# Kernel tuning notes

Measured on AMD Instinct MI355X. Metric: run time of the kernel, lower is better.

The kernel has to match this reference:

```python
import jax, jax.numpy as jnp
import numpy as np

B, T, D = 1, 2048, 2048
NH, DH, DRH, DC = 16, 128, 64, 512


def setup_inputs() -> dict:
    key = jax.random.key(0)
    ks = jax.random.split(key, 12)
    p = lambda k, s: jax.random.normal(k, s, jnp.float32) * 0.02
    h = jax.random.normal(ks[0], (B, T, D), jnp.float32)
    # rotation angles; reference builds complex freqs_cis = cos + i*sin
    freqs_cis = jax.random.uniform(ks[1], (T, DRH // 2), jnp.float32, 0.0, 2.0 * np.pi)
    causal = jnp.tril(jnp.ones((T, T), bool))
    mask = jnp.where(causal, 0.0, -1e9).astype(jnp.float32)
    return {
        "h": h,
        "freqs_cis": freqs_cis,
        "mask": mask,
        "w_dkv": p(ks[2], (DC, D)),
        "w_uk": p(ks[3], (DH, NH, DC)),
        "w_uv": p(ks[4], (DH, NH, DC)),
        "w_dq": p(ks[5], (DC, D)),
        "w_uq": p(ks[6], (DH, NH, DC)),
        "w_qr": p(ks[7], (DRH, NH, DC)),
        "w_kr": p(ks[8], (DRH, D)),
        "w_o": p(ks[9], (D, DH, NH)),
    }


def _rope(x, fc):
    # x: [..., t, drh]; fc: complex [t, drh//2] (broadcasts over leading dims)
    real, imag = jnp.split(x.astype(jnp.float32), 2, -1)
    z = (real + 1j * imag) * fc
    return jnp.concatenate((z.real, z.imag), -1).astype(x.dtype)


def reference(h, freqs_cis, mask, w_dkv, w_uk, w_uv, w_dq, w_uq, w_qr, w_kr, w_o):
    nh, dh, drh = w_uk.shape[1], w_uk.shape[0], w_qr.shape[0]
    fc = jnp.cos(freqs_cis) + 1j * jnp.sin(freqs_cis)  # [t, drh//2] complex
    c_kv = jnp.einsum('cd,btd->btc', w_dkv, h)          # kv latent [b,t,dc]
    k_c = jnp.einsum('enc,btc->bnte', w_uk, c_kv)       # [b,nh,t,dh]
    v_c = jnp.einsum('enc,btc->bnte', w_uv, c_kv)       # [b,nh,t,dh]
    c_q = jnp.einsum('cd,btd->btc', w_dq, h)            # q latent [b,t,dc]
    q_c = jnp.einsum('enc,btc->bnte', w_uq, c_q)        # [b,nh,t,dh]
    q_r = _rope(jnp.einsum('rnc,btc->bntr', w_qr, c_q), fc)  # [b,nh,t,drh]
    k_r = _rope(jnp.einsum('rd,btd->btr', w_kr, h), fc)      # [b,t,drh]
    q = jnp.concatenate((q_c, q_r), -1)                 # [b,nh,t,dh+drh]
    b, t = k_r.shape[0], k_r.shape[1]
    k_r = jnp.broadcast_to(k_r[:, None], (b, nh, t, drh)) / nh
    k = jnp.concatenate((k_c, k_r), -1)                 # [b,nh,t,dh+drh]
    logits = jnp.einsum('bntd,bnld->bntl', q, k) / jnp.sqrt(jnp.float32(dh + drh)) + mask
    scores = jax.nn.softmax(logits.astype(jnp.float32), -1).astype(h.dtype)
    # NOTE: faithful to source: contraction is over the query axis t, output axis is l
    out = jnp.einsum('bntl,bnte->bnle', scores, v_c)    # [b,nh,t,dh] (t named l in src)
    return jnp.einsum('den,bnle->bld', w_o, out)        # [b,t,d]
```

## Files before the change

### kernel.cpp

```cpp
#include <hip/hip_runtime.h>
#include <hip/hip_bf16.h>
#include <math.h>


namespace {

constexpr int T   = 2048;
constexpr int D   = 2048;
constexpr int NH  = 16;
constexpr int DH  = 128;
constexpr int DRH = 64;
constexpr int DC  = 512;
constexpr int QK  = 192;
constexpr float SCL2E = 0.07216878364870322f * 1.4426950408889634f;

constexpr long long PH = 2048LL * 32 * 33;

typedef __attribute__((ext_vector_type(8))) short short8;
typedef __attribute__((ext_vector_type(4))) float f32x4;

#define MFMA16(a, b, c) __builtin_amdgcn_mfma_f32_16x16x32_bf16((a), (b), (c), 0, 0, 0)

__device__ __forceinline__ unsigned short f2b(float x) {
    unsigned u = __float_as_uint(x);
    unsigned r = (u + 0x7FFFu + ((u >> 16) & 1u)) >> 16;
    return (unsigned short)r;
}
__device__ __forceinline__ unsigned short f2bt(float x) {
    return (unsigned short)(__float_as_uint(x) >> 16);
}
__device__ __forceinline__ float b2f(unsigned short s) {
    return __uint_as_float(((unsigned)s) << 16);
}

typedef __attribute__((address_space(1))) const unsigned int* gas_t;
typedef __attribute__((address_space(3))) unsigned int* las_t;
__device__ __forceinline__ void async16(const unsigned short* g, unsigned short* l) {
    __builtin_amdgcn_global_load_lds((gas_t)(const void*)g, (las_t)(void*)l, 16, 0, 0);
}

constexpr long long SZ_H    = (long long)T * D;
constexpr long long SZ_DKV  = (long long)DC * D;
constexpr long long SZ_UK   = (long long)DH * NH * DC;
constexpr long long SZ_UV   = SZ_UK;
constexpr long long SZ_DQ   = SZ_DKV;
constexpr long long SZ_UQ   = SZ_UK;
constexpr long long SZ_QR   = (long long)DRH * NH * DC;
constexpr long long SZ_KR   = (long long)DRH * D;
constexpr long long C0 = SZ_H;
constexpr long long C1 = C0 + SZ_DKV;
constexpr long long C2 = C1 + SZ_UK;
constexpr long long C3 = C2 + SZ_UV;
constexpr long long C4 = C3 + SZ_DQ;
constexpr long long C5 = C4 + SZ_UQ;
constexpr long long C6 = C5 + SZ_QR;
constexpr long long C7 = C6 + SZ_KR;

__global__ __launch_bounds__(256) void cast_all(
    const float* __restrict__ h,   const float* __restrict__ wdkv,
    const float* __restrict__ wuk, const float* __restrict__ wuv,
    const float* __restrict__ wdq, const float* __restrict__ wuq,
    const float* __restrict__ wqr, const float* __restrict__ wkr,
    unsigned short* __restrict__ hb,   unsigned short* __restrict__ dkvb,
    unsigned short* __restrict__ dqb,  unsigned short* __restrict__ ukb,
    unsigned short* __restrict__ uvb,  unsigned short* __restrict__ wqall,
    unsigned short* __restrict__ krb)
{
    long long i4 = ((long long)blockIdx.x * 256 + threadIdx.x) * 4;
    const float* src; unsigned short* dst; long long soff, doff;
    if      (i4 < C0) { src = h;    dst = hb;   soff = i4;      doff = soff; }
    else if (i4 < C1) { src = wdkv; dst = dkvb; soff = i4 - C0; doff = soff; }
    else if (i4 < C2) { src = wuk;  dst = ukb;  soff = i4 - C1; doff = soff; }
    else if (i4 < C3) { src = wuv;  dst = uvb;  soff = i4 - C2; doff = soff; }
    else if (i4 < C4) { src = wdq;  dst = dqb;  soff = i4 - C3; doff = soff; }
    else if (i4 < C5) {
        src = wuq; dst = wqall; soff = i4 - C4;
        long long e = soff >> 13, n = (soff >> 9) & 15, c = soff & 511;
        doff = n * 98304 + e * 512 + c;
    }
    else if (i4 < C6) {
        src = wqr; dst = wqall; soff = i4 - C5;
        long long e = soff >> 13, n = (soff >> 9) & 15, c = soff & 511;
        doff = n * 98304 + (128 + e) * 512 + c;
    }
    else              { src = wkr;  dst = krb;  soff = i4 - C6; doff = soff; }
    float4 v = *(const float4*)(src + soff);
    uint2 pk;
    pk.x = (unsigned)f2b(v.x) | ((unsigned)f2b(v.y) << 16);
    pk.y = (unsigned)f2b(v.z) | ((unsigned)f2b(v.w) << 16);
    *(uint2*)(dst + doff) = pk;
}

__global__ __launch_bounds__(256) void wo_permute(const float* __restrict__ wo,
                                                  unsigned short* __restrict__ wob)
{
    __shared__ float row[2048];
    int d = blockIdx.x;
    const float* src = wo + (long long)d * 2048;
#pragma unroll
    for (int i = 0; i < 8; ++i) row[threadIdx.x + i * 256] = src[threadIdx.x + i * 256];
    __syncthreads();
    unsigned short* dst = wob + (long long)d * 2048;
#pragma unroll
    for (int i = 0; i < 8; ++i) {
        int j = threadIdx.x + i * 256;
        int n = j >> 7, e = j & 127;
        dst[j] = f2b(row[e * 16 + n]);
    }
}

template<int BM, int BN, int WM, int WN, bool OUTB, bool SPLITK = false>
__global__ __launch_bounds__(256) void gemm_bf16(
    const unsigned short* __restrict__ A, const unsigned short* __restrict__ B,
    void* __restrict__ C, int K, int lda, int ldb, int ldc,
    long long sB, long long sC)
{
    constexpr int MT = WM / 16, NT = WN / 16;
    constexpr int WX = BN / WN;
    __shared__ unsigned short As[2][BM * 32];
    __shared__ unsigned short Bs[2][BN * 32];
    const int tid = (int)threadIdx.x;
    const int wave = tid >> 6, lane = tid & 63;
    const int q = lane >> 4, c = lane & 15;
    const int wm = (wave / WX) * WM, wn = (wave % WX) * WN;
    const int m0 = (int)blockIdx.x * BM, n0 = (int)blockIdx.y * BN;

    const unsigned short* Ab;
    const unsigned short* Bb;
    long long cb;
    if constexpr (SPLITK) {
        int koff = (int)blockIdx.z * K;
        Ab = A + koff;
        Bb = B + koff;
        cb = (long long)blockIdx.z * sC;
    } else {
        Ab = A;
        Bb = B + (long long)blockIdx.z * sB;
        cb = (long long)blockIdx.z * sC;
    }

    f32x4 acc[MT][NT];
#pragma unroll
    for (int i = 0; i < MT; ++i)
#pragma unroll
        for (int j = 0; j < NT; ++j) acc[i][j] = (f32x4){0.f, 0.f, 0.f, 0.f};

    auto STAGE = [&](int buf, int k0) {
#pragma unroll
        for (int i = 0; i < BM / 64; ++i) {
            int ch = tid + i * 256;
            async16(&Ab[(long long)(m0 + (ch >> 2)) * lda + k0 + (((ch & 3) ^ ((ch >> 3) & 3)) * 8)],
                    &As[buf][(i * 256 + wave * 64) * 8]);
        }
#pragma unroll
        for (int i = 0; i < BN / 64; ++i) {
            int ch = tid + i * 256;
            async16(&Bb[(long long)(n0 + (ch >> 2)) * ldb + k0 + (((ch & 3) ^ ((ch >> 3) & 3)) * 8)],
                    &Bs[buf][(i * 256 + wave * 64) * 8]);
        }
    };

    STAGE(0, 0);
    __syncthreads();
    int cur = 0;
    for (int k0 = 0; k0 < K; k0 += 32) {
        if (k0 + 32 < K) STAGE(cur ^ 1, k0 + 32);
        short8 af[MT], bfr[NT];
#pragma unroll
        for (int i = 0; i < MT; ++i) {
            int row = wm + i * 16 + c;
            af[i] = *(const short8*)&As[cur][row * 32 + (q ^ ((row >> 1) & 3)) * 8];
        }
#pragma unroll
        for (int j = 0; j < NT; ++j) {
            int row = wn + j * 16 + c;
            bfr[j] = *(const short8*)&Bs[cur][row * 32 + (q ^ ((row >> 1) & 3)) * 8];
        }
#pragma unroll
        for (int i = 0; i < MT; ++i)
#pragma unroll
            for (int j = 0; j < NT; ++j)
                acc[i][j] = MFMA16(af[i], bfr[j], acc[i][j]);
        __syncthreads();
        cur ^= 1;
    }
#pragma unroll
    for (int i = 0; i < MT; ++i)
#pragma unroll
        for (int j = 0; j < NT; ++j) {
            int rbase = m0 + wm + i * 16 + q * 4;
            int col = n0 + wn + j * 16 + c;
#pragma unroll
            for (int rr = 0; rr < 4; ++rr) {
                long long off = cb + (long long)(rbase + rr) * ldc + col;
                if (OUTB) ((unsigned short*)C)[off] = f2b(acc[i][j][rr]);
                else      ((float*)C)[off] = acc[i][j][rr];
            }
        }
}

__global__ __launch_bounds__(256) void rope_q(unsigned short* __restrict__ qh,
                                              const float* __restrict__ fr)
{
    int idx = (int)blockIdx.x * 256 + (int)threadIdx.x;
    int j = idx & 31;
    int t = (idx >> 5) & (T - 1);
    int n = idx >> 16;
    float sn, cs;
    sincosf(fr[t * 32 + j], &sn, &cs);
    long long base = ((long long)(n * T + t)) * QK + 128 + j;
    float x0 = b2f(qh[base]);
    float x1 = b2f(qh[base + 32]);
    qh[base]      = f2b(x0 * cs - x1 * sn);
    qh[base + 32] = f2b(x0 * sn + x1 * cs);
}

__global__ __launch_bounds__(256) void rope_k(const float* __restrict__ krtp,
                                              unsigned short* __restrict__ kh,
                                              const float* __restrict__ fr)
{
    int idx = (int)blockIdx.x * 256 + (int)threadIdx.x;
    int j = idx & 31;
    int t = idx >> 5;
    float sn, cs;
    sincosf(fr[t * 32 + j], &sn, &cs);
    float x0 = 0.f, x1 = 0.f;
#pragma unroll
    for (int pth = 0; pth < 4; ++pth) {
        x0 += krtp[pth * (T * 64) + t * 64 + j];
        x1 += krtp[pth * (T * 64) + t * 64 + 32 + j];
    }
    unsigned short y0 = f2b((x0 * cs - x1 * sn) * (1.0f / 16.0f));
    unsigned short y1 = f2b((x0 * sn + x1 * cs) * (1.0f / 16.0f));
#pragma unroll
    for (int n = 0; n < NH; ++n) {
        long long base = ((long long)(n * T + t)) * QK + 128 + j;
        kh[base]      = y0;
        kh[base + 32] = y1;
    }
}

__global__ __launch_bounds__(256) void vtrans(const unsigned short* __restrict__ vbh,
                                              const float* __restrict__ zrow,
                                              unsigned short* __restrict__ vt)
{
    __shared__ unsigned short ts[32][33];
    __shared__ float zi[32];
    int t0 = (int)blockIdx.x * 32, e0 = (int)blockIdx.y * 32, n = (int)blockIdx.z;
    int tid = (int)threadIdx.x;
    if (tid < 32) zi[tid] = 1.0f / zrow[n * T + t0 + tid];
    int r = tid >> 3, cq = (tid & 7) * 4;
    const unsigned short* src = vbh + ((long long)(n * T + t0 + r)) * DH + e0 + cq;
#pragma unroll
    for (int i = 0; i < 4; ++i) ts[r][cq + i] = src[i];
    __syncthreads();
    unsigned short* dst = vt + ((long long)(n * DH + e0 + r)) * T + t0 + cq;
#pragma unroll
    for (int i = 0; i < 4; ++i) dst[i] = f2b(b2f(ts[cq + i][r]) * zi[cq + i]);
}

__global__ __launch_bounds__(256) void row_stats_p(const unsigned short* __restrict__ qh,
                                                   const unsigned short* __restrict__ kh,
                                                   float* __restrict__ zrow,
                                                   unsigned short* __restrict__ Pbuf)
{
    int id = (int)blockIdx.x;
    int n = (id & 7) * 2 + ((id >> 3) & 1);
    int rest = id >> 4;
    int tbi = 31 - (rest & 31);
    int chunk = rest >> 5;
    int tid = (int)threadIdx.x, wave = tid >> 6, lane = tid & 63;
    int q = lane >> 4, c = lane & 15;
    int tw = tbi * 64 + wave * 16;

    __shared__ unsigned short Ks[64 * 200];

    const unsigned short* qp = qh + ((long long)(n * T + tw + c)) * QK;
    short8 qf[6];
#pragma unroll
    for (int f = 0; f < 6; ++f) qf[f] = *(const short8*)(qp + f * 32 + q * 8);

    float z = 0.f;
    const unsigned short* kbase = kh + (long long)n * T * QK;
    unsigned short* Ph = Pbuf + (long long)n * PH;

    short8 kreg[6];
    int lt = chunk;
    if (lt <= tbi) {
        const unsigned short* kp = kbase + (long long)lt * 64 * QK;
#pragma unroll
        for (int i = 0; i < 6; ++i) {
            int ch = tid + i * 256;
            int r = ch / 24, cc = ch - r * 24;
            kreg[i] = *(const short8*)(kp + r * QK + cc * 8);
        }
    }
    for (; lt <= tbi; lt += 4) {
        __syncthreads();
#pragma unroll
        for (int i = 0; i < 6; ++i) {
            int ch = tid + i * 256;
            int r = ch / 24, cc = ch - r * 24;
            *(short8*)&Ks[r * 200 + cc * 8] = kreg[i];
        }
        __syncthreads();
        if (lt + 4 <= tbi) {
            const unsigned short* kp = kbase + (long long)(lt + 4) * 64 * QK;
#pragma unroll
            for (int i = 0; i < 6; ++i) {
                int ch = tid + i * 256;
                int r = ch / 24, cc = ch - r * 24;
                kreg[i] = *(const short8*)(kp + r * QK + cc * 8);
            }
        }
        f32x4 d[4];
#pragma unroll
        for (int ls = 0; ls < 4; ++ls) d[ls] = (f32x4){0.f, 0.f, 0.f, 0.f};
        __builtin_amdgcn_s_setprio(1);
#pragma unroll
        for (int f = 0; f < 6; ++f)
#pragma unroll
            for (int ls = 0; ls < 4; ++ls) {
                short8 ka = *(const short8*)&Ks[(ls * 16 + c) * 200 + f * 32 + q * 8];
                d[ls] = MFMA16(ka, qf[f], d[ls]);
            }
        __builtin_amdgcn_s_setprio(0);
        int L = T - lt * 64;
        unsigned short* pb = Ph + (long long)2048 * lt * (65 - lt)
                             + (long long)(q * 4) * L + (tbi - lt) * 64 + wave * 16 + c;
        if (lt == tbi) {
            int tl = wave * 16 + c;
#pragma unroll
            for (int ls = 0; ls < 4; ++ls)
#pragma unroll
                for (int r = 0; r < 4; ++r) {
                    float pe = exp2f(d[ls][r] * SCL2E);
                    bool ok = (ls * 16 + q * 4 + r) <= tl;
                    z += ok ? pe : 0.f;
                    pb[(ls * 16 + r) * L] = ok ? f2bt(pe) : (unsigned short)0;
                }
        } else {
#pragma unroll
            for (int ls = 0; ls < 4; ++ls)
#pragma unroll
                for (int r = 0; r < 4; ++r) {
                    float pe = exp2f(d[ls][r] * SCL2E);
                    z += pe;
                    pb[(ls * 16 + r) * L] = f2bt(pe);
                }
        }
    }
    z += __shfl_xor(z, 16);
    z += __shfl_xor(z, 32);
    if (q == 0) atomicAdd(&zrow[n * T + tw + c], z);
}

__global__ __launch_bounds__(256) void pv_gemm(const unsigned short* __restrict__ Pbuf,
                                               const unsigned short* __restrict__ vt,
                                               unsigned short* __restrict__ p0,
                                               unsigned short* __restrict__ p1)
{
    __shared__ unsigned short As[2][64 * 32];
    __shared__ unsigned short Bs[2][128 * 32];
    const int j = (int)blockIdx.x, chunk = (int)blockIdx.y, n = (int)blockIdx.z;
    const int tid = (int)threadIdx.x, wave = tid >> 6, lane = tid & 63;
    const int q = lane >> 4, c = lane & 15;
    const int wm = (wave >> 1) * 32, wn = (wave & 1) * 64;
    const int m0 = j * 64;
    const int L = T - m0;
    const int ntile = 32 - j;
    const unsigned short* A = Pbuf + (long long)n * PH + (long long)2048 * j * (65 - j);
    const unsigned short* B = vt + (long long)n * DH * T + m0;

    f32x4 acc[2][4];
#pragma unroll
    for (int i = 0; i < 2; ++i)
#pragma unroll
        for (int jj = 0; jj < 4; ++jj) acc[i][jj] = (f32x4){0.f, 0.f, 0.f, 0.f};

    const int tcount = (ntile - chunk + 1) >> 1;
    const int nsteps = tcount * 2;

    auto STAGE = [&](int buf, int k0) {
        async16(&A[(long long)(tid >> 2) * L + k0 + (((tid & 3) ^ ((tid >> 3) & 3)) * 8)],
                &As[buf][wave * 512]);
#pragma unroll
        for (int i = 0; i < 2; ++i) {
            int ch = tid + i * 256;
            async16(&B[(long long)(ch >> 2) * T + k0 + (((ch & 3) ^ ((ch >> 3) & 3)) * 8)],
                    &Bs[buf][(i * 256 + wave * 64) * 8]);
        }
    };
    auto K0 = [&](int s) { return (chunk + ((s >> 1) << 1)) * 64 + (s & 1) * 32; };

    if (nsteps > 0) STAGE(0, K0(0));
    __syncthreads();
    int cur = 0;
    for (int s = 0; s < nsteps; ++s) {
        if (s + 1 < nsteps) STAGE(cur ^ 1, K0(s + 1));
        short8 af[2], bfr[4];
#pragma unroll
        for (int i = 0; i < 2; ++i) {
            int row = wm + i * 16 + c;
            af[i] = *(const short8*)&As[cur][row * 32 + (q ^ ((row >> 1) & 3)) * 8];
        }
#pragma unroll
        for (int jj = 0; jj < 4; ++jj) {
            int row = wn + jj * 16 + c;
            bfr[jj] = *(const short8*)&Bs[cur][row * 32 + (q ^ ((row >> 1) & 3)) * 8];
        }
#pragma unroll
        for (int i = 0; i < 2; ++i)
#pragma unroll
            for (int jj = 0; jj < 4; ++jj)
                acc[i][jj] = MFMA16(af[i], bfr[jj], acc[i][jj]);
        __syncthreads();
        cur ^= 1;
    }
    unsigned short* op = chunk ? p1 : p0;
#pragma unroll
    for (int i = 0; i < 2; ++i)
#pragma unroll
        for (int jj = 0; jj < 4; ++jj) {
            int rbase = m0 + wm + i * 16 + q * 4;
            int col = n * 128 + wn + jj * 16 + c;
#pragma unroll
            for (int rr = 0; rr < 4; ++rr)
                op[(long long)(rbase + rr) * D + col] = f2b(acc[i][jj][rr]);
        }
}

__global__ __launch_bounds__(256) void sum_cast2(const unsigned short* __restrict__ a,
                                                 const unsigned short* __restrict__ b,
                                                 unsigned short* __restrict__ o)
{
    long long i = ((long long)blockIdx.x * 256 + threadIdx.x) * 8;
    short8 va = *(const short8*)(a + i);
    short8 vb = *(const short8*)(b + i);
    short8 vo;
#pragma unroll
    for (int j = 0; j < 8; ++j)
        vo[j] = (short)f2b(b2f((unsigned short)va[j]) + b2f((unsigned short)vb[j]));
    *(short8*)(o + i) = vo;
}

}

extern "C" void kernel_launch(void* const* d_in, const int* in_sizes, int n_in,
                              void* d_out, int out_size, void* d_ws, size_t ws_size,
                              hipStream_t stream)
{
    (void)in_sizes; (void)n_in; (void)out_size; (void)ws_size;
    const float* h    = (const float*)d_in[0];
    const float* fr   = (const float*)d_in[1];
    const float* wdkv = (const float*)d_in[3];
    const float* wuk  = (const float*)d_in[4];
    const float* wuv  = (const float*)d_in[5];
    const float* wdq  = (const float*)d_in[6];
    const float* wuq  = (const float*)d_in[7];
    const float* wqr  = (const float*)d_in[8];
    const float* wkr  = (const float*)d_in[9];
    const float* wo   = (const float*)d_in[10];
    float* out = (float*)d_out;

    char* p = (char*)d_ws;
    auto alloc = [&](long long bytes) { char* r = p; p += (bytes + 255) & ~255LL; return r; };
    unsigned short* qhb   = (unsigned short*)alloc((long long)NH * T * QK * 2);
    unsigned short* khb   = (unsigned short*)alloc((long long)NH * T * QK * 2);
    unsigned short* vbh   = (unsigned short*)alloc((long long)NH * T * DH * 2);
    float*          zrow  = (float*)alloc((long long)NH * T * 4);
    unsigned short* vtb   = (unsigned short*)alloc((long long)NH * T * DH * 2);
    unsigned short* Pbuf  = (unsigned short*)alloc(PH * NH * 2);
    char* q = (char*)Pbuf;
    auto sub = [&](long long bytes) { char* r = q; q += (bytes + 255) & ~255LL; return r; };
    unsigned short* hb    = (unsigned short*)sub(SZ_H * 2);
    unsigned short* dkvb  = (unsigned short*)sub(SZ_DKV * 2);
    unsigned short* dqb   = (unsigned short*)sub(SZ_DQ * 2);
    unsigned short* ukb   = (unsigned short*)sub(SZ_UK * 2);
    unsigned short* uvb   = (unsigned short*)sub(SZ_UV * 2);
    unsigned short* wqall = (unsigned short*)sub((SZ_UQ + SZ_QR) * 2);
    unsigned short* krb   = (unsigned short*)sub(SZ_KR * 2);
    unsigned short* ckvq  = (unsigned short*)sub((long long)T * 1024 * 2);
    float*          krt   = (float*)sub((long long)T * DRH * 4 * 4);
    unsigned short* attn2 = vbh;
    unsigned short* wob   = vtb;
    unsigned short* pvp0  = qhb;
    unsigned short* pvp1  = khb;

    cast_all<<<dim3((unsigned)(C7 / 1024)), 256, 0, stream>>>(
        h, wdkv, wuk, wuv, wdq, wuq, wqr, wkr, hb, dkvb, dqb, ukb, uvb, wqall, krb);

    gemm_bf16<64,128,32,64,true><<<dim3(T/64, 1024/128, 1), 256, 0, stream>>>(
        hb, dkvb, ckvq, D, D, D, 1024, 0, 0);
    gemm_bf16<64,64,32,32,false,true><<<dim3(T/64, 1, 4), 256, 0, stream>>>(
        hb, krb, krt, D/4, D, D, DRH, 0, (long long)T * DRH);
    gemm_bf16<64,128,32,64,true><<<dim3(T/64, 1, NH), 256, 0, stream>>>(
        ckvq, ukb, khb, DC, 1024, NH*DC, QK, DC, (long long)T * QK);
    gemm_bf16<64,128,32,64,true><<<dim3(T/64, 1, NH), 256, 0, stream>>>(
        ckvq, uvb, vbh, DC, 1024, NH*DC, DH, DC, (long long)T * DH);
    gemm_bf16<128,64,32,64,true><<<dim3(T/128, 3, NH), 256, 0, stream>>>(
        ckvq + DC, wqall, qhb, DC, 1024, DC, QK, (long long)192 * DC, (long long)T * QK);

    rope_q<<<dim3(NH * T * 32 / 256), 256, 0, stream>>>(qhb, fr);
    rope_k<<<dim3(T * 32 / 256), 256, 0, stream>>>(krt, khb, fr);

    hipMemsetAsync(zrow, 0, (long long)NH * T * 4, stream);
    row_stats_p<<<dim3(2048), 256, 0, stream>>>(qhb, khb, zrow, Pbuf);
    vtrans<<<dim3(T/32, DH/32, NH), 256, 0, stream>>>(vbh, zrow, vtb);
    pv_gemm<<<dim3(32, 2, NH), 256, 0, stream>>>(Pbuf, vtb, pvp0, pvp1);
    sum_cast2<<<dim3(T * D / 2048), 256, 0, stream>>>(pvp0, pvp1, attn2);

    wo_permute<<<dim3(D), 256, 0, stream>>>(wo, wob);
    gemm_bf16<64,128,32,64,false><<<dim3(T/64, D/128, 1), 256, 0, stream>>>(
        attn2, wob, out, D, D, D, D, 0, 0);
}
```

Measured before the change: 340.3 us.

## Pair short and long causal tiles per block for balanced score and PV work

Both the score/P kernel and the PV GEMM now give each block a pair of row tiles (pr and 31-pr), so every block does about the same amount of causal-triangle work. The score kernel splits the key tiles into 6 strided chunks instead of 4 and the PV GEMM into 4 chunks instead of 2, with grids of 1536 and 1024 blocks. The PV partial results now go to four buffers, one of them newly allocated, and are summed by a four-input cast kernel. This adds some workspace and extra partial-sum traffic in exchange for less tail imbalance across the causal triangle.

```diff
diff --git a/kernel.cpp b/kernel.cpp
--- a/kernel.cpp
+++ b/kernel.cpp
@@ -267,45 +267,31 @@
     int id = (int)blockIdx.x;
     int n = (id & 7) * 2 + ((id >> 3) & 1);
     int rest = id >> 4;
-    int tbi = 31 - (rest & 31);
-    int chunk = rest >> 5;
+    int pr = rest & 15;
+    int chunk = rest >> 4;
     int tid = (int)threadIdx.x, wave = tid >> 6, lane = tid & 63;
     int q = lane >> 4, c = lane & 15;
-    int tw = tbi * 64 + wave * 16;
 
     __shared__ unsigned short Ks[64 * 200];
 
-    const unsigned short* qp = qh + ((long long)(n * T + tw + c)) * QK;
-    short8 qf[6];
-#pragma unroll
-    for (int f = 0; f < 6; ++f) qf[f] = *(const short8*)(qp + f * 32 + q * 8);
-
-    float z = 0.f;
     const unsigned short* kbase = kh + (long long)n * T * QK;
     unsigned short* Ph = Pbuf + (long long)n * PH;
 
-    short8 kreg[6];
-    int lt = chunk;
-    if (lt <= tbi) {
-        const unsigned short* kp = kbase + (long long)lt * 64 * QK;
-#pragma unroll
-        for (int i = 0; i < 6; ++i) {
-            int ch = tid + i * 256;
-            int r = ch / 24, cc = ch - r * 24;
-            kreg[i] = *(const short8*)(kp + r * QK + cc * 8);
-        }
-    }
-    for (; lt <= tbi; lt += 4) {
-        __syncthreads();
-#pragma unroll
-        for (int i = 0; i < 6; ++i) {
-            int ch = tid + i * 256;
-            int r = ch / 24, cc = ch - r * 24;
-            *(short8*)&Ks[r * 200 + cc * 8] = kreg[i];
-        }
-        __syncthreads();
-        if (lt + 4 <= tbi) {
-            const unsigned short* kp = kbase + (long long)(lt + 4) * 64 * QK;
+#pragma unroll
+    for (int ph = 0; ph < 2; ++ph) {
+        int tbi = ph ? pr : 31 - pr;
+        int tw = tbi * 64 + wave * 16;
+
+        const unsigned short* qp = qh + ((long long)(n * T + tw + c)) * QK;
+        short8 qf[6];
+#pragma unroll
+        for (int f = 0; f < 6; ++f) qf[f] = *(const short8*)(qp + f * 32 + q * 8);
+
+        float z = 0.f;
+        short8 kreg[6];
+        int lt = chunk;
+        if (lt <= tbi) {
+            const unsigned short* kp = kbase + (long long)lt * 64 * QK;
 #pragma unroll
             for (int i = 0; i < 6; ++i) {
                 int ch = tid + i * 256;
@@ -313,134 +299,169 @@
                 kreg[i] = *(const short8*)(kp + r * QK + cc * 8);
             }
         }
-        f32x4 d[4];
-#pragma unroll
-        for (int ls = 0; ls < 4; ++ls) d[ls] = (f32x4){0.f, 0.f, 0.f, 0.f};
-        __builtin_amdgcn_s_setprio(1);
-#pragma unroll
-        for (int f = 0; f < 6; ++f)
-#pragma unroll
-            for (int ls = 0; ls < 4; ++ls) {
-                short8 ka = *(const short8*)&Ks[(ls * 16 + c) * 200 + f * 32 + q * 8];
-                d[ls] = MFMA16(ka, qf[f], d[ls]);
-            }
-        __builtin_amdgcn_s_setprio(0);
-        int L = T - lt * 64;
-        unsigned short* pb = Ph + (long long)2048 * lt * (65 - lt)
-                             + (long long)(q * 4) * L + (tbi - lt) * 64 + wave * 16 + c;
-        if (lt == tbi) {
-            int tl = wave * 16 + c;
-#pragma unroll
-            for (int ls = 0; ls < 4; ++ls)
-#pragma unroll
-                for (int r = 0; r < 4; ++r) {
-                    float pe = exp2f(d[ls][r] * SCL2E);
-                    bool ok = (ls * 16 + q * 4 + r) <= tl;
-                    z += ok ? pe : 0.f;
-                    pb[(ls * 16 + r) * L] = ok ? f2bt(pe) : (unsigned short)0;
+        for (; lt <= tbi; lt += 6) {
+            __syncthreads();
+#pragma unroll
+            for (int i = 0; i < 6; ++i) {
+                int ch = tid + i * 256;
+                int r = ch / 24, cc = ch - r * 24;
+                *(short8*)&Ks[r * 200 + cc * 8] = kreg[i];
+            }
+            __syncthreads();
+            if (lt + 6 <= tbi) {
+                const unsigned short* kp = kbase + (long long)(lt + 6) * 64 * QK;
+#pragma unroll
+                for (int i = 0; i < 6; ++i) {
+                    int ch = tid + i * 256;
+                    int r = ch / 24, cc = ch - r * 24;
+                    kreg[i] = *(const short8*)(kp + r * QK + cc * 8);
                 }
-        } else {
-#pragma unroll
-            for (int ls = 0; ls < 4; ++ls)
-#pragma unroll
-                for (int r = 0; r < 4; ++r) {
-                    float pe = exp2f(d[ls][r] * SCL2E);
-                    z += pe;
-                    pb[(ls * 16 + r) * L] = f2bt(pe);
+            }
+            f32x4 d[4];
+#pragma unroll
+            for (int ls = 0; ls < 4; ++ls) d[ls] = (f32x4){0.f, 0.f, 0.f, 0.f};
+            __builtin_amdgcn_s_setprio(1);
+#pragma unroll
+            for (int f = 0; f < 6; ++f)
+#pragma unroll
+                for (int ls = 0; ls < 4; ++ls) {
+                    short8 ka = *(const short8*)&Ks[(ls * 16 + c) * 200 + f * 32 + q * 8];
+                    d[ls] = MFMA16(ka, qf[f], d[ls]);
                 }
-        }
-    }
-    z += __shfl_xor(z, 16);
-    z += __shfl_xor(z, 32);
-    if (q == 0) atomicAdd(&zrow[n * T + tw + c], z);
+            __builtin_amdgcn_s_setprio(0);
+            int L = T - lt * 64;
+            unsigned short* pb = Ph + (long long)2048 * lt * (65 - lt)
+                                 + (long long)(q * 4) * L + (tbi - lt) * 64 + wave * 16 + c;
+            if (lt == tbi) {
+                int tl = wave * 16 + c;
+#pragma unroll
+                for (int ls = 0; ls < 4; ++ls)
+#pragma unroll
+                    for (int r = 0; r < 4; ++r) {
+                        float pe = exp2f(d[ls][r] * SCL2E);
+                        bool ok = (ls * 16 + q * 4 + r) <= tl;
+                        z += ok ? pe : 0.f;
+                        pb[(ls * 16 + r) * L] = ok ? f2bt(pe) : (unsigned short)0;
+                    }
+            } else {
+#pragma unroll
+                for (int ls = 0; ls < 4; ++ls)
+#pragma unroll
+                    for (int r = 0; r < 4; ++r) {
+                        float pe = exp2f(d[ls][r] * SCL2E);
+                        z += pe;
+                        pb[(ls * 16 + r) * L] = f2bt(pe);
+                    }
+            }
+        }
+        z += __shfl_xor(z, 16);
+        z += __shfl_xor(z, 32);
+        if (q == 0) atomicAdd(&zrow[n * T + tw + c], z);
+    }
 }
 
 __global__ __launch_bounds__(256) void pv_gemm(const unsigned short* __restrict__ Pbuf,
                                                const unsigned short* __restrict__ vt,
                                                unsigned short* __restrict__ p0,
-                                               unsigned short* __restrict__ p1)
+                                               unsigned short* __restrict__ p1,
+                                               unsigned short* __restrict__ p2,
+                                               unsigned short* __restrict__ p3)
 {
     __shared__ unsigned short As[2][64 * 32];
     __shared__ unsigned short Bs[2][128 * 32];
-    const int j = (int)blockIdx.x, chunk = (int)blockIdx.y, n = (int)blockIdx.z;
+    int id = (int)blockIdx.x;
+    int n = (id & 7) * 2 + ((id >> 3) & 1);
+    int rest = id >> 4;
+    int pr = rest & 15;
+    int chunk = rest >> 4;
     const int tid = (int)threadIdx.x, wave = tid >> 6, lane = tid & 63;
     const int q = lane >> 4, c = lane & 15;
     const int wm = (wave >> 1) * 32, wn = (wave & 1) * 64;
-    const int m0 = j * 64;
-    const int L = T - m0;
-    const int ntile = 32 - j;
-    const unsigned short* A = Pbuf + (long long)n * PH + (long long)2048 * j * (65 - j);
-    const unsigned short* B = vt + (long long)n * DH * T + m0;
-
-    f32x4 acc[2][4];
-#pragma unroll
-    for (int i = 0; i < 2; ++i)
-#pragma unroll
-        for (int jj = 0; jj < 4; ++jj) acc[i][jj] = (f32x4){0.f, 0.f, 0.f, 0.f};
-
-    const int tcount = (ntile - chunk + 1) >> 1;
-    const int nsteps = tcount * 2;
-
-    auto STAGE = [&](int buf, int k0) {
-        async16(&A[(long long)(tid >> 2) * L + k0 + (((tid & 3) ^ ((tid >> 3) & 3)) * 8)],
-                &As[buf][wave * 512]);
-#pragma unroll
-        for (int i = 0; i < 2; ++i) {
-            int ch = tid + i * 256;
-            async16(&B[(long long)(ch >> 2) * T + k0 + (((ch & 3) ^ ((ch >> 3) & 3)) * 8)],
-                    &Bs[buf][(i * 256 + wave * 64) * 8]);
-        }
-    };
-    auto K0 = [&](int s) { return (chunk + ((s >> 1) << 1)) * 64 + (s & 1) * 32; };
-
-    if (nsteps > 0) STAGE(0, K0(0));
-    __syncthreads();
-    int cur = 0;
-    for (int s = 0; s < nsteps; ++s) {
-        if (s + 1 < nsteps) STAGE(cur ^ 1, K0(s + 1));
-        short8 af[2], bfr[4];
-#pragma unroll
-        for (int i = 0; i < 2; ++i) {
-            int row = wm + i * 16 + c;
-            af[i] = *(const short8*)&As[cur][row * 32 + (q ^ ((row >> 1) & 3)) * 8];
-        }
-#pragma unroll
-        for (int jj = 0; jj < 4; ++jj) {
-            int row = wn + jj * 16 + c;
-            bfr[jj] = *(const short8*)&Bs[cur][row * 32 + (q ^ ((row >> 1) & 3)) * 8];
-        }
+    unsigned short* op = (chunk == 0) ? p0 : (chunk == 1) ? p1 : (chunk == 2) ? p2 : p3;
+
+#pragma unroll
+    for (int ph = 0; ph < 2; ++ph) {
+        int j = ph ? (31 - pr) : pr;
+        int m0 = j * 64;
+        int L = T - m0;
+        int ntile = 32 - j;
+        const unsigned short* A = Pbuf + (long long)n * PH + (long long)2048 * j * (65 - j);
+        const unsigned short* B = vt + (long long)n * DH * T + m0;
+
+        f32x4 acc[2][4];
 #pragma unroll
         for (int i = 0; i < 2; ++i)
 #pragma unroll
-            for (int jj = 0; jj < 4; ++jj)
-                acc[i][jj] = MFMA16(af[i], bfr[jj], acc[i][jj]);
+            for (int jj = 0; jj < 4; ++jj) acc[i][jj] = (f32x4){0.f, 0.f, 0.f, 0.f};
+
+        int tcnt = (chunk < ntile) ? (((ntile - 1 - chunk) >> 2) + 1) : 0;
+        int nsteps = tcnt * 2;
+
+        auto STAGE = [&](int buf, int k0) {
+            async16(&A[(long long)(tid >> 2) * L + k0 + (((tid & 3) ^ ((tid >> 3) & 3)) * 8)],
+                    &As[buf][wave * 512]);
+#pragma unroll
+            for (int i = 0; i < 2; ++i) {
+                int ch = tid + i * 256;
+                async16(&B[(long long)(ch >> 2) * T + k0 + (((ch & 3) ^ ((ch >> 3) & 3)) * 8)],
+                        &Bs[buf][(i * 256 + wave * 64) * 8]);
+            }
+        };
+        auto K0 = [&](int s) { return (chunk + ((s >> 1) << 2)) * 64 + (s & 1) * 32; };
+
+        if (nsteps > 0) STAGE(0, K0(0));
         __syncthreads();
-        cur ^= 1;
-    }
-    unsigned short* op = chunk ? p1 : p0;
-#pragma unroll
-    for (int i = 0; i < 2; ++i)
-#pragma unroll
-        for (int jj = 0; jj < 4; ++jj) {
-            int rbase = m0 + wm + i * 16 + q * 4;
-            int col = n * 128 + wn + jj * 16 + c;
-#pragma unroll
-            for (int rr = 0; rr < 4; ++rr)
-                op[(long long)(rbase + rr) * D + col] = f2b(acc[i][jj][rr]);
-        }
-}
-
-__global__ __launch_bounds__(256) void sum_cast2(const unsigned short* __restrict__ a,
-                                                 const unsigned short* __restrict__ b,
-                                                 unsigned short* __restrict__ o)
+        int cur = 0;
+        for (int s = 0; s < nsteps; ++s) {
+            if (s + 1 < nsteps) STAGE(cur ^ 1, K0(s + 1));
+            short8 af[2], bfr[4];
+#pragma unroll
+            for (int i = 0; i < 2; ++i) {
+                int row = wm + i * 16 + c;
+                af[i] = *(const short8*)&As[cur][row * 32 + (q ^ ((row >> 1) & 3)) * 8];
+            }
+#pragma unroll
+            for (int jj = 0; jj < 4; ++jj) {
+                int row = wn + jj * 16 + c;
+                bfr[jj] = *(const short8*)&Bs[cur][row * 32 + (q ^ ((row >> 1) & 3)) * 8];
+            }
+#pragma unroll
+            for (int i = 0; i < 2; ++i)
+#pragma unroll
+                for (int jj = 0; jj < 4; ++jj)
+                    acc[i][jj] = MFMA16(af[i], bfr[jj], acc[i][jj]);
+            __syncthreads();
+            cur ^= 1;
+        }
+#pragma unroll
+        for (int i = 0; i < 2; ++i)
+#pragma unroll
+            for (int jj = 0; jj < 4; ++jj) {
+                int rbase = m0 + wm + i * 16 + q * 4;
+                int col = n * 128 + wn + jj * 16 + c;
+#pragma unroll
+                for (int rr = 0; rr < 4; ++rr)
+                    op[(long long)(rbase + rr) * D + col] = f2b(acc[i][jj][rr]);
+            }
+    }
+}
+
+__global__ __launch_bounds__(256) void sum_cast4(const unsigned short* a,
+                                                 const unsigned short* b,
+                                                 const unsigned short* cc_,
+                                                 const unsigned short* dd_,
+                                                 unsigned short* o)
 {
     long long i = ((long long)blockIdx.x * 256 + threadIdx.x) * 8;
     short8 va = *(const short8*)(a + i);
     short8 vb = *(const short8*)(b + i);
+    short8 vc = *(const short8*)(cc_ + i);
+    short8 vd = *(const short8*)(dd_ + i);
     short8 vo;
 #pragma unroll
     for (int j = 0; j < 8; ++j)
-        vo[j] = (short)f2b(b2f((unsigned short)va[j]) + b2f((unsigned short)vb[j]));
+        vo[j] = (short)f2b((b2f((unsigned short)va[j]) + b2f((unsigned short)vb[j])) +
+                           (b2f((unsigned short)vc[j]) + b2f((unsigned short)vd[j])));
     *(short8*)(o + i) = vo;
 }
 
@@ -470,6 +491,7 @@
     unsigned short* vbh   = (unsigned short*)alloc((long long)NH * T * DH * 2);
     float*          zrow  = (float*)alloc((long long)NH * T * 4);
     unsigned short* vtb   = (unsigned short*)alloc((long long)NH * T * DH * 2);
+    unsigned short* pv3   = (unsigned short*)alloc((long long)T * D * 2);
     unsigned short* Pbuf  = (unsigned short*)alloc(PH * NH * 2);
     char* q = (char*)Pbuf;
     auto sub = [&](long long bytes) { char* r = q; q += (bytes + 255) & ~255LL; return r; };
@@ -482,10 +504,12 @@
     unsigned short* krb   = (unsigned short*)sub(SZ_KR * 2);
     unsigned short* ckvq  = (unsigned short*)sub((long long)T * 1024 * 2);
     float*          krt   = (float*)sub((long long)T * DRH * 4 * 4);
-    unsigned short* attn2 = vbh;
-    unsigned short* wob   = vtb;
     unsigned short* pvp0  = qhb;
     unsigned short* pvp1  = khb;
+    unsigned short* pvp2  = vbh;
+    unsigned short* pvp3  = pv3;
+    unsigned short* attn2 = pvp0;
+    unsigned short* wob   = vtb;
 
     cast_all<<<dim3((unsigned)(C7 / 1024)), 256, 0, stream>>>(
         h, wdkv, wuk, wuv, wdq, wuq, wqr, wkr, hb, dkvb, dqb, ukb, uvb, wqall, krb);
@@ -505,10 +529,10 @@
     rope_k<<<dim3(T * 32 / 256), 256, 0, stream>>>(krt, khb, fr);
 
     hipMemsetAsync(zrow, 0, (long long)NH * T * 4, stream);
-    row_stats_p<<<dim3(2048), 256, 0, stream>>>(qhb, khb, zrow, Pbuf);
+    row_stats_p<<<dim3(1536), 256, 0, stream>>>(qhb, khb, zrow, Pbuf);
     vtrans<<<dim3(T/32, DH/32, NH), 256, 0, stream>>>(vbh, zrow, vtb);
-    pv_gemm<<<dim3(32, 2, NH), 256, 0, stream>>>(Pbuf, vtb, pvp0, pvp1);
-    sum_cast2<<<dim3(T * D / 2048), 256, 0, stream>>>(pvp0, pvp1, attn2);
+    pv_gemm<<<dim3(1024), 256, 0, stream>>>(Pbuf, vtb, pvp0, pvp1, pvp2, pvp3);
+    sum_cast4<<<dim3(T * D / 2048), 256, 0, stream>>>(pvp0, pvp1, pvp2, pvp3, attn2);
 
     wo_permute<<<dim3(D), 256, 0, stream>>>(wo, wob);
     gemm_bf16<64,128,32,64,false><<<dim3(T/64, D/128, 1), 256, 0, stream>>>(
```

New measurement: 322.1 us. 1.06x faster.
